# Kernel optimization log

Measured on AMD Instinct MI355X. Metric: run time of the kernel, lower is better.

## Reference

```python
import jax, jax.numpy as jnp
import numpy as np
from jax import lax

B, C, H, W = 4, 256, 64, 64
K = 9          # points
G = 32         # GroupNorm groups
EPS = 1e-5


def base_offset():
    # matches get_base_offset: y = 0, x in [-(K-1)//2 .. K//2], interleaved (y,x)
    bx = jnp.arange(-((K - 1) // 2), K // 2 + 1, dtype=jnp.float32)
    by = jnp.zeros_like(bx)
    return jnp.stack([by, bx], axis=1).reshape(1, 2 * K, 1, 1)


def conv3x3(x, w, b):
    y = lax.conv_general_dilated(x, w, (1, 1), ((1, 1), (1, 1)),
                                 dimension_numbers=('NCHW', 'OIHW', 'NCHW'))
    return y + b[None, :, None, None]


def group_norm(x, gamma, beta):
    b, c, h, w = x.shape
    xg = x.reshape(b, G, c // G, h, w)
    mu = xg.mean(axis=(2, 3, 4), keepdims=True)
    var = xg.var(axis=(2, 3, 4), keepdims=True)
    xn = ((xg - mu) * lax.rsqrt(var + EPS)).reshape(b, c, h, w)
    return xn * gamma[None, :, None, None] + beta[None, :, None, None]


def _deform_sample_one(img, off):
    # img: [C,H,W]; off: [K,2,H,W] (y,x). Kernel [1,K], stride 1, pad (0, K//2).
    c, h, w = img.shape
    base_x = (jnp.arange(K) - K // 2).astype(img.dtype)  # kernel grid x positions
    py = off[:, 0] + jnp.arange(h, dtype=img.dtype)[None, :, None]                 # [K,H,W]
    px = off[:, 1] + jnp.arange(w, dtype=img.dtype)[None, None, :] + base_x[:, None, None]
    y0 = jnp.floor(py)
    x0 = jnp.floor(px)
    wy = py - y0
    wx = px - x0
    flat = img.reshape(c, h * w)

    def corner(yi, xi):
        valid = (yi >= 0) & (yi <= h - 1) & (xi >= 0) & (xi <= w - 1)
        yc = jnp.clip(yi, 0, h - 1).astype(jnp.int32)
        xc = jnp.clip(xi, 0, w - 1).astype(jnp.int32)
        v = flat[:, (yc * w + xc).reshape(-1)].reshape(c, K, h, w)
        return v * valid[None].astype(img.dtype)

    return (corner(y0, x0) * ((1 - wy) * (1 - wx))[None]
            + corner(y0, x0 + 1) * ((1 - wy) * wx)[None]
            + corner(y0 + 1, x0) * (wy * (1 - wx))[None]
            + corner(y0 + 1, x0 + 1) * (wy * wx)[None])  # [C,K,H,W]


def deform_conv(x, offset, w):
    # x [B,C,H,W]; offset [B,2K,H,W]; w [O,C,1,K]; no bias (mmcv DeformConv2d)
    b, _, h, ww = x.shape
    off = offset.reshape(b, K, 2, h, ww)
    cols = jax.vmap(_deform_sample_one)(x, off)  # [B,C,K,H,W]
    return jnp.einsum('bckhw,ock->bohw', cols, w[:, :, 0, :])


def setup_inputs() -> dict:
    key = jax.random.key(0)
    ks = jax.random.split(key, 8)
    return {
        'cls_feat': jax.random.normal(ks[0], (B, C, H, W), jnp.float32),
        'reg_feat': jax.random.normal(ks[1], (B, C, H, W), jnp.float32),
        'offc_w': jax.random.normal(ks[2], (C, C, 3, 3), jnp.float32) * 0.01,
        'offc_b': jnp.zeros((C,), jnp.float32),
        'offc_g': jnp.ones((C,), jnp.float32),
        'offc_bt': jnp.zeros((C,), jnp.float32),
        'offo_w': jax.random.normal(ks[3], (2 * K, C, 3, 3), jnp.float32) * 0.01,
        'offo_b': jnp.zeros((2 * K,), jnp.float32),
        'clsdc_w': jax.random.normal(ks[4], (C, C, 1, K), jnp.float32) / np.sqrt(C * K),
        'cls_g': jnp.ones((C,), jnp.float32),
        'cls_bt': jnp.zeros((C,), jnp.float32),
        'regdc_w': jax.random.normal(ks[5], (C, C, 1, K), jnp.float32) / np.sqrt(C * K),
        'reg_g': jnp.ones((C,), jnp.float32),
        'reg_bt': jnp.zeros((C,), jnp.float32),
    }


def reference(cls_feat, reg_feat, offc_w, offc_b, offc_g, offc_bt,
              offo_w, offo_b, clsdc_w, cls_g, cls_bt, regdc_w, reg_g, reg_bt):
    # offset branch: ConvModule(3x3) -> GN -> ReLU, then 3x3 offset_out head
    t = jax.nn.relu(group_norm(conv3x3(reg_feat, offc_w, offc_b), offc_g, offc_bt))
    pts = conv3x3(t, offo_w, offo_b)          # [B, 2K, H, W]
    off = pts - base_offset()
    cls_out = jax.nn.relu(group_norm(deform_conv(cls_feat, off, clsdc_w), cls_g, cls_bt))
    reg_out = jax.nn.relu(group_norm(deform_conv(reg_feat, off, regdc_w), reg_g, reg_bt))
    return pts, cls_out, reg_out
```

## Files before the change

### kernel.cpp

```cpp
#include <hip/hip_runtime.h>
#include <math.h>

#define BB 4
#define CC 256
#define HH 64
#define WW 64
#define KP 9
#define GG 32
#define HWW (HH*WW)
#define FEL ((size_t)BB*CC*HH*WW)
#define GN_CNT 32768.0f

typedef __bf16 bf16x8 __attribute__((ext_vector_type(8)));
typedef float  f32x4  __attribute__((ext_vector_type(4)));

__device__ __forceinline__ float bflo(unsigned u) {
    union { unsigned u; float f; } x; x.u = u << 16; return x.f;
}
__device__ __forceinline__ float bfhi(unsigned u) {
    union { unsigned u; float f; } x; x.u = u & 0xffff0000u; return x.f;
}

#define VT256_RD(row, P)  (((row) << 8) + ((((P) ^ ((row) & 7))) << 3))
#define VT256_WR(row, u)  (((row) << 8) + (((((u) >> 1) ^ ((row) & 7))) << 3) + (((u) & 1) << 2))
#define VT128_RD(row, P)  (((row) << 7) + ((((P) ^ ((row) & 7))) << 3))
#define VT128_WR(row, u)  (((row) << 7) + (((((u) >> 1) ^ ((row) & 7))) << 3) + (((u) & 1) << 2))

__global__ void prep_all(const float* __restrict__ w1, const float* __restrict__ wc,
                         const float* __restrict__ wr, const float* __restrict__ w18,
                         __bf16* __restrict__ f1, __bf16* __restrict__ fc,
                         __bf16* __restrict__ fr, __bf16* __restrict__ f18,
                         float* __restrict__ stats) {
    int gid = blockIdx.x * 256 + threadIdx.x;
    if (gid < 768) stats[gid] = 0.f;
    const int NW = 589824;
    if (gid < 3 * NW) {
        int which = gid / NW;
        int idx = gid - which * NW;
        int j   = idx & 7;
        int l   = (idx >> 3) & 63;
        int o16 = (idx >> 9) & 15;
        int c0  = (idx >> 13) & 7;
        int k   = idx >> 16;
        int o = o16 * 16 + (l & 15);
        int c = c0 * 32 + (l >> 4) * 8 + j;
        const float* src = (which == 0) ? w1 : ((which == 1) ? wc : wr);
        __bf16* dst = (which == 0) ? f1 : ((which == 1) ? fc : fr);
        dst[idx] = (__bf16)src[(size_t)(o * 256 + c) * 9 + k];
    } else {
        int idx = gid - 3 * NW;
        int j   = idx & 7;
        int l   = (idx >> 3) & 63;
        int o16 = (idx >> 9) & 1;
        int c0  = (idx >> 10) & 7;
        int k   = idx >> 13;
        int o = o16 * 16 + (l & 15);
        int c = c0 * 32 + (l >> 4) * 8 + j;
        float v = (o < 18) ? w18[(size_t)(o * 256 + c) * 9 + k] : 0.f;
        f18[idx] = (__bf16)v;
    }
}

__global__ void transpose_feat(const float* __restrict__ cls,
                               const float* __restrict__ reg,
                               __bf16* __restrict__ out_cls,
                               __bf16* __restrict__ out_reg) {
    __shared__ float tile[64][65];
    int c0 = blockIdx.x * 64;
    int y  = blockIdx.y;
    int b  = blockIdx.z & 3;
    const float* in = (blockIdx.z >> 2) ? reg : cls;
    __bf16* out     = (blockIdx.z >> 2) ? out_reg : out_cls;
    int lx = threadIdx.x & 63;
    int q  = threadIdx.x >> 6;
    for (int j = 0; j < 16; ++j) {
        int ci = q * 16 + j;
        tile[ci][lx] = in[(((size_t)b*CC + c0 + ci)*HH + y)*WW + lx];
    }
    __syncthreads();
    for (int j = 0; j < 16; ++j) {
        int xi = q * 16 + j;
        out[(((size_t)b*HH + y)*WW + xi)*CC + c0 + lx] = (__bf16)tile[lx][xi];
    }
}

__global__ __launch_bounds__(256, 2) void conv1_mfma(
    const __bf16* __restrict__ in_cl,
    const __bf16* __restrict__ wf,
    const float* __restrict__ bias,
    __bf16* __restrict__ t_out,
    float* __restrict__ stats)
{
    __shared__ __bf16 Vt[66 * 256];
    __shared__ float groupStats[64];
    int blk = blockIdx.x;
    int bb = blk & 3;
    int oh = (blk >> 2) & 1;
    int y  = blk >> 3;
    int t  = threadIdx.x;
    int w  = t >> 6;
    int l  = t & 63;
    int quad = l >> 4;
    int l15  = l & 15;
    if (t < 64) groupStats[t] = 0.f;

    const __bf16* inb = in_cl + (size_t)bb * HWW * CC;
    f32x4 acc[4][2];
    #pragma unroll
    for (int i = 0; i < 4; ++i)
        #pragma unroll
        for (int j = 0; j < 2; ++j)
            acc[i][j] = (f32x4){0.f, 0.f, 0.f, 0.f};

    for (int ky = 0; ky < 3; ++ky) {
        int yy = y + ky - 1;
        bool yok = (yy >= 0 && yy < HH);
        __syncthreads();
        for (int u = t; u < 66 * 64; u += 256) {
            int xl = u >> 6, cu = u & 63;
            int gx = xl - 1;
            uint2 val = make_uint2(0u, 0u);
            if (yok && gx >= 0 && gx < WW)
                val = *(const uint2*)(inb + ((size_t)(yy * WW + gx)) * CC + cu * 4);
            *(uint2*)&Vt[VT256_WR(xl, cu)] = val;
        }
        __syncthreads();
        #pragma unroll
        for (int kx = 0; kx < 3; ++kx) {
            int k = ky * 3 + kx;
            const bf16x8* wbase = (const bf16x8*)(wf + (size_t)k * 65536);
            for (int c0 = 0; c0 < 8; ++c0) {
                bf16x8 a[4], bfr[2];
                #pragma unroll
                for (int pt = 0; pt < 4; ++pt) {
                    int row = pt * 16 + l15 + kx;
                    a[pt] = *(const bf16x8*)&Vt[VT256_RD(row, c0 * 4 + quad)];
                }
                #pragma unroll
                for (int ot = 0; ot < 2; ++ot)
                    bfr[ot] = wbase[(c0 * 16 + (oh * 8 + w * 2 + ot)) * 64 + l];
                #pragma unroll
                for (int pt = 0; pt < 4; ++pt)
                    #pragma unroll
                    for (int ot = 0; ot < 2; ++ot)
                        acc[pt][ot] = __builtin_amdgcn_mfma_f32_16x16x32_bf16(
                            a[pt], bfr[ot], acc[pt][ot], 0, 0, 0);
            }
        }
    }
    #pragma unroll
    for (int ot = 0; ot < 2; ++ot) {
        int o = oh * 128 + w * 32 + ot * 16 + l15;
        float bi = bias[o];
        float s1 = 0.f, s2 = 0.f;
        #pragma unroll
        for (int pt = 0; pt < 4; ++pt)
            #pragma unroll
            for (int r = 0; r < 4; ++r) {
                float v = acc[pt][ot][r] + bi;
                int px = pt * 16 + quad * 4 + r;
                t_out[(((size_t)bb * HH + y) * WW + px) * CC + o] = (__bf16)v;
                s1 += v; s2 += v * v;
            }
        s1 += __shfl_xor(s1, 16, 64); s1 += __shfl_xor(s1, 32, 64);
        s2 += __shfl_xor(s2, 16, 64); s2 += __shfl_xor(s2, 32, 64);
        if (quad == 0) {
            atomicAdd(&groupStats[(o >> 3) * 2],     s1);
            atomicAdd(&groupStats[(o >> 3) * 2 + 1], s2);
        }
    }
    __syncthreads();
    if (t < 64) atomicAdd(&stats[bb * 64 + t], groupStats[t]);
}

__global__ __launch_bounds__(256, 2) void conv18_mfma(
    const __bf16* __restrict__ t_bf,
    const __bf16* __restrict__ wf18,
    const float* __restrict__ bias,
    const float* __restrict__ stats,
    const float* __restrict__ gamma, const float* __restrict__ beta,
    float* __restrict__ pts)
{
    __shared__ __bf16 Vt[66 * 256];
    int blk = blockIdx.x;
    int bb = blk & 3;
    int y  = blk >> 2;
    int t  = threadIdx.x;
    int w  = t >> 6;
    int l  = t & 63;
    int quad = l >> 4;
    int l15  = l & 15;
    const __bf16* inb = t_bf + (size_t)bb * HWW * CC;

    int cbase = (t & 63) * 4;
    int g = cbase >> 3;
    float mu = stats[bb * 64 + g * 2]     * (1.f / GN_CNT);
    float ms = stats[bb * 64 + g * 2 + 1] * (1.f / GN_CNT);
    float rs = rsqrtf(ms - mu * mu + 1e-5f);
    float sc[4], sh[4];
    #pragma unroll
    for (int j = 0; j < 4; ++j) {
        float ga = gamma[cbase + j];
        sc[j] = rs * ga;
        sh[j] = beta[cbase + j] - mu * rs * ga;
    }

    f32x4 acc[2];
    acc[0] = (f32x4){0.f, 0.f, 0.f, 0.f};
    acc[1] = (f32x4){0.f, 0.f, 0.f, 0.f};

    for (int ky = 0; ky < 3; ++ky) {
        int yy = y + ky - 1;
        bool yok = (yy >= 0 && yy < HH);
        __syncthreads();
        for (int u = t; u < 66 * 64; u += 256) {
            int xl = u >> 6, cu = u & 63;
            int gx = xl - 1;
            uint2 val = make_uint2(0u, 0u);
            if (yok && gx >= 0 && gx < WW) {
                uint2 q = *(const uint2*)(inb + ((size_t)(yy * WW + gx)) * CC + cu * 4);
                float v0 = fmaxf(bflo(q.x) * sc[0] + sh[0], 0.f);
                float v1 = fmaxf(bfhi(q.x) * sc[1] + sh[1], 0.f);
                float v2 = fmaxf(bflo(q.y) * sc[2] + sh[2], 0.f);
                float v3 = fmaxf(bfhi(q.y) * sc[3] + sh[3], 0.f);
                __bf16 o4[4] = {(__bf16)v0, (__bf16)v1, (__bf16)v2, (__bf16)v3};
                val = *(const uint2*)o4;
            }
            *(uint2*)&Vt[VT256_WR(xl, cu)] = val;
        }
        __syncthreads();
        #pragma unroll
        for (int kx = 0; kx < 3; ++kx) {
            int k = ky * 3 + kx;
            const bf16x8* wbase = (const bf16x8*)(wf18 + (size_t)k * 8192);
            for (int c0 = 0; c0 < 8; ++c0) {
                int row = w * 16 + l15 + kx;
                bf16x8 a = *(const bf16x8*)&Vt[VT256_RD(row, c0 * 4 + quad)];
                #pragma unroll
                for (int o16 = 0; o16 < 2; ++o16) {
                    bf16x8 bfr = wbase[(c0 * 2 + o16) * 64 + l];
                    acc[o16] = __builtin_amdgcn_mfma_f32_16x16x32_bf16(a, bfr, acc[o16], 0, 0, 0);
                }
            }
        }
    }
    #pragma unroll
    for (int o16 = 0; o16 < 2; ++o16) {
        int o = o16 * 16 + l15;
        if (o < 18) {
            float bi = bias[o];
            float4 st;
            st.x = acc[o16][0] + bi;
            st.y = acc[o16][1] + bi;
            st.z = acc[o16][2] + bi;
            st.w = acc[o16][3] + bi;
            *(float4*)(pts + (((size_t)bb*18 + o)*HH + y)*WW + w*16 + quad*4) = st;
        }
    }
}

__global__ __launch_bounds__(256, 2) void deform_mfma(
    const __bf16* __restrict__ cls_cl, const __bf16* __restrict__ reg_cl,
    const __bf16* __restrict__ wfc, const __bf16* __restrict__ wfr,
    const float* __restrict__ pts,
    __bf16* __restrict__ out_cls, __bf16* __restrict__ out_reg,
    float* __restrict__ stats)
{
    __shared__ float pairW4[576 * 4];
    __shared__ int   pairO4[576 * 4];
    __shared__ __bf16 Vt[2][64 * 128];
    __shared__ float groupStats[64];

    int blk = blockIdx.x;
    int g8  = blk & 7;
    int which = g8 & 1;
    int bb  = g8 >> 1;
    int y   = blk >> 3;
    const __bf16* featb = (which ? reg_cl : cls_cl) + (size_t)bb * HWW * CC;
    const __bf16* wf    = which ? wfr : wfc;
    __bf16* outp  = which ? out_reg : out_cls;
    float* statsP = stats + 256 + which * 256 + bb * 64;

    int t = threadIdx.x;
    int w = t >> 6;
    int l = t & 63;
    int quad = l >> 4;
    int l15  = l & 15;
    int lh   = l >> 5;
    int cq   = l & 31;

    if (t < 64) groupStats[t] = 0.f;
    for (int j = t; j < 576; j += 256) {
        int k = j >> 6;
        int x = j & 63;
        float py  = pts[(((size_t)bb*18 + 2*k)*HH + y)*WW + x] + (float)y;
        float pxf = pts[(((size_t)bb*18 + 2*k + 1)*HH + y)*WW + x] + (float)x;
        float y0f = floorf(py), x0f = floorf(pxf);
        float wy = py - y0f, wx = pxf - x0f;
        int iy0 = (int)y0f, ix0 = (int)x0f;
        int iy1 = iy0 + 1,  ix1 = ix0 + 1;
        bool vy0 = (iy0 >= 0 && iy0 < HH), vy1 = (iy1 >= 0 && iy1 < HH);
        bool vx0 = (ix0 >= 0 && ix0 < WW), vx1 = (ix1 >= 0 && ix1 < WW);
        int cy0 = min(max(iy0, 0), HH-1), cy1 = min(max(iy1, 0), HH-1);
        int cx0 = min(max(ix0, 0), WW-1), cx1 = min(max(ix1, 0), WW-1);
        pairW4[j*4+0] = (1.f-wy)*(1.f-wx) * ((vy0 && vx0) ? 1.f : 0.f);
        pairW4[j*4+1] = (1.f-wy)*wx       * ((vy0 && vx1) ? 1.f : 0.f);
        pairW4[j*4+2] = wy*(1.f-wx)       * ((vy1 && vx0) ? 1.f : 0.f);
        pairW4[j*4+3] = wy*wx             * ((vy1 && vx1) ? 1.f : 0.f);
        pairO4[j*4+0] = (cy0*WW + cx0)*CC;
        pairO4[j*4+1] = (cy0*WW + cx1)*CC;
        pairO4[j*4+2] = (cy1*WW + cx0)*CC;
        pairO4[j*4+3] = (cy1*WW + cx1)*CC;
    }

    f32x4 acc[4][4];
    #pragma unroll
    for (int i = 0; i < 4; ++i)
        #pragma unroll
        for (int j = 0; j < 4; ++j)
            acc[i][j] = (f32x4){0.f, 0.f, 0.f, 0.f};

    auto sample2 = [&](int s, int u) {
        int k = s >> 1, ch = s & 1;
        __bf16* buf = &Vt[s & 1][0];
        const __bf16* fb = featb + ch * 128 + cq * 4;
        #pragma unroll
        for (int it2 = 0; it2 < 2; ++it2) {
            int pxi = w * 16 + (u * 2 + it2) * 2 + lh;
            int j = k * 64 + pxi;
            float4 wv = *(const float4*)&pairW4[j * 4];
            int4   ov = *(const int4*)&pairO4[j * 4];
            uint2 q00 = *(const uint2*)(fb + ov.x);
            uint2 q01 = *(const uint2*)(fb + ov.y);
            uint2 q10 = *(const uint2*)(fb + ov.z);
            uint2 q11 = *(const uint2*)(fb + ov.w);
            float v0 = wv.x*bflo(q00.x) + wv.y*bflo(q01.x) + wv.z*bflo(q10.x) + wv.w*bflo(q11.x);
            float v1 = wv.x*bfhi(q00.x) + wv.y*bfhi(q01.x) + wv.z*bfhi(q10.x) + wv.w*bfhi(q11.x);
            float v2 = wv.x*bflo(q00.y) + wv.y*bflo(q01.y) + wv.z*bflo(q10.y) + wv.w*bflo(q11.y);
            float v3 = wv.x*bfhi(q00.y) + wv.y*bfhi(q01.y) + wv.z*bfhi(q10.y) + wv.w*bfhi(q11.y);
            __bf16 o4[4] = {(__bf16)v0, (__bf16)v1, (__bf16)v2, (__bf16)v3};
            *(uint2*)&buf[VT128_WR(pxi, cq)] = *(const uint2*)o4;
        }
    };
    auto mfma4 = [&](int s, int u) {
        int k = s >> 1, ch = s & 1;
        const __bf16* buf = &Vt[s & 1][0];
        const bf16x8* wbase = (const bf16x8*)(wf + (size_t)k * 65536);
        int c0g = ch * 4 + u;
        bf16x8 a[4], bfr[4];
        #pragma unroll
        for (int pt = 0; pt < 4; ++pt)
            a[pt] = *(const bf16x8*)&buf[VT128_RD(pt * 16 + l15, u * 4 + quad)];
        #pragma unroll
        for (int ot = 0; ot < 4; ++ot)
            bfr[ot] = wbase[(c0g * 16 + (w * 4 + ot)) * 64 + l];
        #pragma unroll
        for (int ot = 0; ot < 4; ++ot)
            #pragma unroll
            for (int pt = 0; pt < 4; ++pt)
                acc[ot][pt] = __builtin_amdgcn_mfma_f32_16x16x32_bf16(
                    bfr[ot], a[pt], acc[ot][pt], 0, 0, 0);
    };

    __syncthreads();
    #pragma unroll
    for (int u = 0; u < 4; ++u) sample2(0, u);
    #pragma unroll 1
    for (int s = 1; s < 18; ++s) {
        __syncthreads();
        #pragma unroll
        for (int u = 0; u < 4; ++u) {
            sample2(s, u);
            mfma4(s - 1, u);
        }
    }
    __syncthreads();
    #pragma unroll
    for (int u = 0; u < 4; ++u) mfma4(17, u);

    #pragma unroll
    for (int ot = 0; ot < 4; ++ot)
        #pragma unroll
        for (int r = 0; r < 4; ++r) {
            int o = w * 64 + ot * 16 + quad * 4 + r;
            __bf16* orow = outp + ((size_t)(bb*CC + o))*HWW + y*WW + l15;
            float s1 = 0.f, s2 = 0.f;
            #pragma unroll
            for (int pt = 0; pt < 4; ++pt) {
                float v = acc[ot][pt][r];
                orow[pt * 16] = (__bf16)v;
                s1 += v; s2 += v * v;
            }
            s1 += __shfl_xor(s1, 1, 64); s1 += __shfl_xor(s1, 2, 64);
            s1 += __shfl_xor(s1, 4, 64); s1 += __shfl_xor(s1, 8, 64);
            s2 += __shfl_xor(s2, 1, 64); s2 += __shfl_xor(s2, 2, 64);
            s2 += __shfl_xor(s2, 4, 64); s2 += __shfl_xor(s2, 8, 64);
            if (l15 == 0) {
                atomicAdd(&groupStats[(o >> 3) * 2],     s1);
                atomicAdd(&groupStats[(o >> 3) * 2 + 1], s2);
            }
        }
    __syncthreads();
    if (t < 64) atomicAdd(&statsP[t], groupStats[t]);
}

__global__ void gn_relu_nchw(const __bf16* __restrict__ in_cls, const __bf16* __restrict__ in_reg,
                             float* __restrict__ out_cls, float* __restrict__ out_reg,
                             const float* __restrict__ stats_base,
                             const float* __restrict__ gcls, const float* __restrict__ bcls,
                             const float* __restrict__ greg, const float* __restrict__ breg) {
    int which = blockIdx.y;
    const __bf16* in = which ? in_reg  : in_cls;
    float* out       = which ? out_reg : out_cls;
    const float* st  = stats_base + (which ? 512 : 256);
    const float* gg  = which ? greg : gcls;
    const float* be  = which ? breg : bcls;
    size_t e = ((size_t)blockIdx.x * 256 + threadIdx.x) * 8;
    int c = (int)((e >> 12) & 255);
    int b = (int)(e >> 20);
    int g = c >> 3;
    float mu = st[(b*32 + g)*2] * (1.f / GN_CNT);
    float ms = st[(b*32 + g)*2 + 1] * (1.f / GN_CNT);
    float rs = rsqrtf(ms - mu*mu + 1e-5f);
    float ga = gg[c], bb = be[c];
    uint4 q = *(const uint4*)(in + e);
    float v[8] = {bflo(q.x), bfhi(q.x), bflo(q.y), bfhi(q.y),
                  bflo(q.z), bfhi(q.z), bflo(q.w), bfhi(q.w)};
    float4 r0, r1;
    r0.x = fmaxf((v[0] - mu)*rs*ga + bb, 0.f);
    r0.y = fmaxf((v[1] - mu)*rs*ga + bb, 0.f);
    r0.z = fmaxf((v[2] - mu)*rs*ga + bb, 0.f);
    r0.w = fmaxf((v[3] - mu)*rs*ga + bb, 0.f);
    r1.x = fmaxf((v[4] - mu)*rs*ga + bb, 0.f);
    r1.y = fmaxf((v[5] - mu)*rs*ga + bb, 0.f);
    r1.z = fmaxf((v[6] - mu)*rs*ga + bb, 0.f);
    r1.w = fmaxf((v[7] - mu)*rs*ga + bb, 0.f);
    *(float4*)(out + e)     = r0;
    *(float4*)(out + e + 4) = r1;
}

extern "C" void kernel_launch(void* const* d_in, const int* in_sizes, int n_in,
                              void* d_out, int out_size, void* d_ws, size_t ws_size,
                              hipStream_t stream) {
    (void)in_sizes; (void)n_in; (void)out_size; (void)ws_size;
    const float* cls_feat = (const float*)d_in[0];
    const float* reg_feat = (const float*)d_in[1];
    const float* offc_w   = (const float*)d_in[2];
    const float* offc_b   = (const float*)d_in[3];
    const float* offc_g   = (const float*)d_in[4];
    const float* offc_bt  = (const float*)d_in[5];
    const float* offo_w   = (const float*)d_in[6];
    const float* offo_b   = (const float*)d_in[7];
    const float* clsdc_w  = (const float*)d_in[8];
    const float* cls_g    = (const float*)d_in[9];
    const float* cls_bt   = (const float*)d_in[10];
    const float* regdc_w  = (const float*)d_in[11];
    const float* reg_g    = (const float*)d_in[12];
    const float* reg_bt   = (const float*)d_in[13];
    float* out = (float*)d_out;

    char* ws = (char*)d_ws;
    __bf16* reg_cl = (__bf16*)ws;
    __bf16* cls_cl = (__bf16*)(ws + 8388608);
    __bf16* t_bf   = (__bf16*)(ws + 16777216);
    __bf16* dc_cls = (__bf16*)(ws + 25165824);
    __bf16* dc_reg = (__bf16*)(ws + 33554432);
    __bf16* wt1f   = (__bf16*)(ws + 41943040);
    __bf16* wtcf   = (__bf16*)(ws + 41943040 + 1179648);
    __bf16* wtrf   = (__bf16*)(ws + 41943040 + 2359296);
    __bf16* wf18   = (__bf16*)(ws + 41943040 + 3538944);
    float*  stats  = (float*)(ws + 41943040 + 3686400);

    float* pts     = out;
    float* out_cls = out + 294912;
    float* out_reg = out + 294912 + FEL;

    hipLaunchKernelGGL(prep_all, dim3(7200), dim3(256), 0, stream,
                       offc_w, clsdc_w, regdc_w, offo_w, wt1f, wtcf, wtrf, wf18, stats);
    hipLaunchKernelGGL(transpose_feat, dim3(4, 64, 8), dim3(256), 0, stream,
                       cls_feat, reg_feat, cls_cl, reg_cl);
    hipLaunchKernelGGL(conv1_mfma, dim3(512), dim3(256), 0, stream,
                       reg_cl, wt1f, offc_b, t_bf, stats);
    hipLaunchKernelGGL(conv18_mfma, dim3(256), dim3(256), 0, stream,
                       t_bf, wf18, offo_b, stats, offc_g, offc_bt, pts);
    hipLaunchKernelGGL(deform_mfma, dim3(512), dim3(256), 0, stream,
                       cls_cl, reg_cl, wtcf, wtrf, pts, dc_cls, dc_reg, stats);
    hipLaunchKernelGGL(gn_relu_nchw, dim3(2048, 2), dim3(256), 0, stream,
                       dc_cls, dc_reg, out_cls, out_reg,
                       stats, cls_g, cls_bt, reg_g, reg_bt);
}
```

Measured before the change: 282.1 us.

## Split conv and deform kernels across more blocks/waves and software-pipeline deform gathers

Conv1 now gives each block one 64-channel output quarter instead of a half, doubling the grid and cutting accumulators so occupancy can rise. Conv18 splits each row into two 32-pixel halves with a smaller LDS tile. The deform kernel moves to 512 threads, with each wave owning 32 output channels. Its sampling is restructured so all gather loads for the next stage are issued before the MFMAs of the current stage, to hide gather latency. In exchange, weight fragments are reloaded across more blocks and more registers are held live for the prefetched gathers.

```diff
diff --git a/kernel.cpp b/kernel.cpp
--- a/kernel.cpp
+++ b/kernel.cpp
@@ -84,7 +84,7 @@
     }
 }
 
-__global__ __launch_bounds__(256, 2) void conv1_mfma(
+__global__ __launch_bounds__(256, 4) void conv1_mfma(
     const __bf16* __restrict__ in_cl,
     const __bf16* __restrict__ wf,
     const float* __restrict__ bias,
@@ -95,8 +95,8 @@
     __shared__ float groupStats[64];
     int blk = blockIdx.x;
     int bb = blk & 3;
-    int oh = (blk >> 2) & 1;
-    int y  = blk >> 3;
+    int oq = (blk >> 2) & 3;
+    int y  = blk >> 4;
     int t  = threadIdx.x;
     int w  = t >> 6;
     int l  = t & 63;
@@ -105,12 +105,9 @@
     if (t < 64) groupStats[t] = 0.f;
 
     const __bf16* inb = in_cl + (size_t)bb * HWW * CC;
-    f32x4 acc[4][2];
+    f32x4 acc[4];
     #pragma unroll
-    for (int i = 0; i < 4; ++i)
-        #pragma unroll
-        for (int j = 0; j < 2; ++j)
-            acc[i][j] = (f32x4){0.f, 0.f, 0.f, 0.f};
+    for (int i = 0; i < 4; ++i) acc[i] = (f32x4){0.f, 0.f, 0.f, 0.f};
 
     for (int ky = 0; ky < 3; ++ky) {
         int yy = y + ky - 1;
@@ -130,34 +127,29 @@
             int k = ky * 3 + kx;
             const bf16x8* wbase = (const bf16x8*)(wf + (size_t)k * 65536);
             for (int c0 = 0; c0 < 8; ++c0) {
-                bf16x8 a[4], bfr[2];
+                bf16x8 a[4];
                 #pragma unroll
                 for (int pt = 0; pt < 4; ++pt) {
                     int row = pt * 16 + l15 + kx;
                     a[pt] = *(const bf16x8*)&Vt[VT256_RD(row, c0 * 4 + quad)];
                 }
-                #pragma unroll
-                for (int ot = 0; ot < 2; ++ot)
-                    bfr[ot] = wbase[(c0 * 16 + (oh * 8 + w * 2 + ot)) * 64 + l];
+                bf16x8 bfr = wbase[(c0 * 16 + (oq * 4 + w)) * 64 + l];
                 #pragma unroll
                 for (int pt = 0; pt < 4; ++pt)
-                    #pragma unroll
-                    for (int ot = 0; ot < 2; ++ot)
-                        acc[pt][ot] = __builtin_amdgcn_mfma_f32_16x16x32_bf16(
-                            a[pt], bfr[ot], acc[pt][ot], 0, 0, 0);
-            }
-        }
-    }
-    #pragma unroll
-    for (int ot = 0; ot < 2; ++ot) {
-        int o = oh * 128 + w * 32 + ot * 16 + l15;
+                    acc[pt] = __builtin_amdgcn_mfma_f32_16x16x32_bf16(
+                        a[pt], bfr, acc[pt], 0, 0, 0);
+            }
+        }
+    }
+    {
+        int o = oq * 64 + w * 16 + l15;
         float bi = bias[o];
         float s1 = 0.f, s2 = 0.f;
         #pragma unroll
         for (int pt = 0; pt < 4; ++pt)
             #pragma unroll
             for (int r = 0; r < 4; ++r) {
-                float v = acc[pt][ot][r] + bi;
+                float v = acc[pt][r] + bi;
                 int px = pt * 16 + quad * 4 + r;
                 t_out[(((size_t)bb * HH + y) * WW + px) * CC + o] = (__bf16)v;
                 s1 += v; s2 += v * v;
@@ -173,7 +165,7 @@
     if (t < 64) atomicAdd(&stats[bb * 64 + t], groupStats[t]);
 }
 
-__global__ __launch_bounds__(256, 2) void conv18_mfma(
+__global__ __launch_bounds__(256, 4) void conv18_mfma(
     const __bf16* __restrict__ t_bf,
     const __bf16* __restrict__ wf18,
     const float* __restrict__ bias,
@@ -181,15 +173,19 @@
     const float* __restrict__ gamma, const float* __restrict__ beta,
     float* __restrict__ pts)
 {
-    __shared__ __bf16 Vt[66 * 256];
+    __shared__ __bf16 Vt[34 * 256];
     int blk = blockIdx.x;
     int bb = blk & 3;
-    int y  = blk >> 2;
+    int xh = (blk >> 2) & 1;
+    int y  = blk >> 3;
     int t  = threadIdx.x;
     int w  = t >> 6;
     int l  = t & 63;
     int quad = l >> 4;
     int l15  = l & 15;
+    int mt   = w & 1;
+    int o16  = w >> 1;
+    int x0   = xh * 32;
     const __bf16* inb = t_bf + (size_t)bb * HWW * CC;
 
     int cbase = (t & 63) * 4;
@@ -205,17 +201,15 @@
         sh[j] = beta[cbase + j] - mu * rs * ga;
     }
 
-    f32x4 acc[2];
-    acc[0] = (f32x4){0.f, 0.f, 0.f, 0.f};
-    acc[1] = (f32x4){0.f, 0.f, 0.f, 0.f};
+    f32x4 acc = (f32x4){0.f, 0.f, 0.f, 0.f};
 
     for (int ky = 0; ky < 3; ++ky) {
         int yy = y + ky - 1;
         bool yok = (yy >= 0 && yy < HH);
         __syncthreads();
-        for (int u = t; u < 66 * 64; u += 256) {
+        for (int u = t; u < 34 * 64; u += 256) {
             int xl = u >> 6, cu = u & 63;
-            int gx = xl - 1;
+            int gx = x0 - 1 + xl;
             uint2 val = make_uint2(0u, 0u);
             if (yok && gx >= 0 && gx < WW) {
                 uint2 q = *(const uint2*)(inb + ((size_t)(yy * WW + gx)) * CC + cu * 4);
@@ -234,32 +228,28 @@
             int k = ky * 3 + kx;
             const bf16x8* wbase = (const bf16x8*)(wf18 + (size_t)k * 8192);
             for (int c0 = 0; c0 < 8; ++c0) {
-                int row = w * 16 + l15 + kx;
+                int row = mt * 16 + l15 + kx;
                 bf16x8 a = *(const bf16x8*)&Vt[VT256_RD(row, c0 * 4 + quad)];
-                #pragma unroll
-                for (int o16 = 0; o16 < 2; ++o16) {
-                    bf16x8 bfr = wbase[(c0 * 2 + o16) * 64 + l];
-                    acc[o16] = __builtin_amdgcn_mfma_f32_16x16x32_bf16(a, bfr, acc[o16], 0, 0, 0);
-                }
-            }
-        }
-    }
-    #pragma unroll
-    for (int o16 = 0; o16 < 2; ++o16) {
+                bf16x8 bfr = wbase[(c0 * 2 + o16) * 64 + l];
+                acc = __builtin_amdgcn_mfma_f32_16x16x32_bf16(a, bfr, acc, 0, 0, 0);
+            }
+        }
+    }
+    {
         int o = o16 * 16 + l15;
         if (o < 18) {
             float bi = bias[o];
             float4 st;
-            st.x = acc[o16][0] + bi;
-            st.y = acc[o16][1] + bi;
-            st.z = acc[o16][2] + bi;
-            st.w = acc[o16][3] + bi;
-            *(float4*)(pts + (((size_t)bb*18 + o)*HH + y)*WW + w*16 + quad*4) = st;
-        }
-    }
-}
-
-__global__ __launch_bounds__(256, 2) void deform_mfma(
+            st.x = acc[0] + bi;
+            st.y = acc[1] + bi;
+            st.z = acc[2] + bi;
+            st.w = acc[3] + bi;
+            *(float4*)(pts + (((size_t)bb*18 + o)*HH + y)*WW + x0 + mt*16 + quad*4) = st;
+        }
+    }
+}
+
+__global__ __launch_bounds__(512, 4) void deform_mfma(
     const __bf16* __restrict__ cls_cl, const __bf16* __restrict__ reg_cl,
     const __bf16* __restrict__ wfc, const __bf16* __restrict__ wfr,
     const float* __restrict__ pts,
@@ -286,11 +276,11 @@
     int l = t & 63;
     int quad = l >> 4;
     int l15  = l & 15;
-    int lh   = l >> 5;
-    int cq   = l & 31;
+    int tp   = t >> 5;
+    int cq   = t & 31;
 
     if (t < 64) groupStats[t] = 0.f;
-    for (int j = t; j < 576; j += 256) {
+    for (int j = t; j < 576; j += 512) {
         int k = j >> 6;
         int x = j & 63;
         float py  = pts[(((size_t)bb*18 + 2*k)*HH + y)*WW + x] + (float)y;
@@ -313,76 +303,87 @@
         pairO4[j*4+3] = (cy1*WW + cx1)*CC;
     }
 
-    f32x4 acc[4][4];
+    f32x4 acc[2][4];
     #pragma unroll
-    for (int i = 0; i < 4; ++i)
+    for (int i = 0; i < 2; ++i)
         #pragma unroll
         for (int j = 0; j < 4; ++j)
             acc[i][j] = (f32x4){0.f, 0.f, 0.f, 0.f};
 
-    auto sample2 = [&](int s, int u) {
+    auto stage_loads = [&](int s, uint2 L[4][4], float4 WV[4]) {
         int k = s >> 1, ch = s & 1;
+        const __bf16* fb = featb + ch * 128 + cq * 4;
+        #pragma unroll
+        for (int it = 0; it < 4; ++it) {
+            int pxi = it * 16 + tp;
+            int j = k * 64 + pxi;
+            WV[it] = *(const float4*)&pairW4[j * 4];
+            int4 ov = *(const int4*)&pairO4[j * 4];
+            L[it][0] = *(const uint2*)(fb + ov.x);
+            L[it][1] = *(const uint2*)(fb + ov.y);
+            L[it][2] = *(const uint2*)(fb + ov.z);
+            L[it][3] = *(const uint2*)(fb + ov.w);
+        }
+    };
+    auto stage_combine = [&](int s, uint2 L[4][4], float4 WV[4]) {
         __bf16* buf = &Vt[s & 1][0];
-        const __bf16* fb = featb + ch * 128 + cq * 4;
-        #pragma unroll
-        for (int it2 = 0; it2 < 2; ++it2) {
-            int pxi = w * 16 + (u * 2 + it2) * 2 + lh;
-            int j = k * 64 + pxi;
-            float4 wv = *(const float4*)&pairW4[j * 4];
-            int4   ov = *(const int4*)&pairO4[j * 4];
-            uint2 q00 = *(const uint2*)(fb + ov.x);
-            uint2 q01 = *(const uint2*)(fb + ov.y);
-            uint2 q10 = *(const uint2*)(fb + ov.z);
-            uint2 q11 = *(const uint2*)(fb + ov.w);
-            float v0 = wv.x*bflo(q00.x) + wv.y*bflo(q01.x) + wv.z*bflo(q10.x) + wv.w*bflo(q11.x);
-            float v1 = wv.x*bfhi(q00.x) + wv.y*bfhi(q01.x) + wv.z*bfhi(q10.x) + wv.w*bfhi(q11.x);
-            float v2 = wv.x*bflo(q00.y) + wv.y*bflo(q01.y) + wv.z*bflo(q10.y) + wv.w*bflo(q11.y);
-            float v3 = wv.x*bfhi(q00.y) + wv.y*bfhi(q01.y) + wv.z*bfhi(q10.y) + wv.w*bfhi(q11.y);
+        #pragma unroll
+        for (int it = 0; it < 4; ++it) {
+            int pxi = it * 16 + tp;
+            float4 wv = WV[it];
+            float v0 = wv.x*bflo(L[it][0].x) + wv.y*bflo(L[it][1].x) + wv.z*bflo(L[it][2].x) + wv.w*bflo(L[it][3].x);
+            float v1 = wv.x*bfhi(L[it][0].x) + wv.y*bfhi(L[it][1].x) + wv.z*bfhi(L[it][2].x) + wv.w*bfhi(L[it][3].x);
+            float v2 = wv.x*bflo(L[it][0].y) + wv.y*bflo(L[it][1].y) + wv.z*bflo(L[it][2].y) + wv.w*bflo(L[it][3].y);
+            float v3 = wv.x*bfhi(L[it][0].y) + wv.y*bfhi(L[it][1].y) + wv.z*bfhi(L[it][2].y) + wv.w*bfhi(L[it][3].y);
             __bf16 o4[4] = {(__bf16)v0, (__bf16)v1, (__bf16)v2, (__bf16)v3};
             *(uint2*)&buf[VT128_WR(pxi, cq)] = *(const uint2*)o4;
         }
     };
-    auto mfma4 = [&](int s, int u) {
+    auto stage_mfma = [&](int s) {
         int k = s >> 1, ch = s & 1;
         const __bf16* buf = &Vt[s & 1][0];
         const bf16x8* wbase = (const bf16x8*)(wf + (size_t)k * 65536);
-        int c0g = ch * 4 + u;
-        bf16x8 a[4], bfr[4];
-        #pragma unroll
-        for (int pt = 0; pt < 4; ++pt)
-            a[pt] = *(const bf16x8*)&buf[VT128_RD(pt * 16 + l15, u * 4 + quad)];
-        #pragma unroll
-        for (int ot = 0; ot < 4; ++ot)
-            bfr[ot] = wbase[(c0g * 16 + (w * 4 + ot)) * 64 + l];
-        #pragma unroll
-        for (int ot = 0; ot < 4; ++ot)
+        #pragma unroll
+        for (int u = 0; u < 4; ++u) {
+            int c0g = ch * 4 + u;
+            bf16x8 a[4], bfr[2];
             #pragma unroll
             for (int pt = 0; pt < 4; ++pt)
-                acc[ot][pt] = __builtin_amdgcn_mfma_f32_16x16x32_bf16(
-                    bfr[ot], a[pt], acc[ot][pt], 0, 0, 0);
+                a[pt] = *(const bf16x8*)&buf[VT128_RD(pt * 16 + l15, u * 4 + quad)];
+            #pragma unroll
+            for (int ot = 0; ot < 2; ++ot)
+                bfr[ot] = wbase[(c0g * 16 + (w * 2 + ot)) * 64 + l];
+            #pragma unroll
+            for (int ot = 0; ot < 2; ++ot)
+                #pragma unroll
+                for (int pt = 0; pt < 4; ++pt)
+                    acc[ot][pt] = __builtin_amdgcn_mfma_f32_16x16x32_bf16(
+                        bfr[ot], a[pt], acc[ot][pt], 0, 0, 0);
+        }
     };
 
     __syncthreads();
-    #pragma unroll
-    for (int u = 0; u < 4; ++u) sample2(0, u);
+    {
+        uint2 L[4][4]; float4 WV[4];
+        stage_loads(0, L, WV);
+        stage_combine(0, L, WV);
+    }
     #pragma unroll 1
     for (int s = 1; s < 18; ++s) {
         __syncthreads();
-        #pragma unroll
-        for (int u = 0; u < 4; ++u) {
-            sample2(s, u);
-            mfma4(s - 1, u);
-        }
+        uint2 L[4][4]; float4 WV[4];
+        stage_loads(s, L, WV);
+        stage_mfma(s - 1);
+        stage_combine(s, L, WV);
     }
     __syncthreads();
+    stage_mfma(17);
+
     #pragma unroll
-    for (int u = 0; u < 4; ++u) mfma4(17, u);
-
-    #pragma unroll
-    for (int ot = 0; ot < 4; ++ot)
+    for (int ot = 0; ot < 2; ++ot)
         #pragma unroll
         for (int r = 0; r < 4; ++r) {
-            int o = w * 64 + ot * 16 + quad * 4 + r;
+            int o = w * 32 + ot * 16 + quad * 4 + r;
             __bf16* orow = outp + ((size_t)(bb*CC + o))*HWW + y*WW + l15;
             float s1 = 0.f, s2 = 0.f;
             #pragma unroll
@@ -479,11 +480,11 @@
                        offc_w, clsdc_w, regdc_w, offo_w, wt1f, wtcf, wtrf, wf18, stats);
     hipLaunchKernelGGL(transpose_feat, dim3(4, 64, 8), dim3(256), 0, stream,
                        cls_feat, reg_feat, cls_cl, reg_cl);
-    hipLaunchKernelGGL(conv1_mfma, dim3(512), dim3(256), 0, stream,
+    hipLaunchKernelGGL(conv1_mfma, dim3(1024), dim3(256), 0, stream,
                        reg_cl, wt1f, offc_b, t_bf, stats);
-    hipLaunchKernelGGL(conv18_mfma, dim3(256), dim3(256), 0, stream,
+    hipLaunchKernelGGL(conv18_mfma, dim3(512), dim3(256), 0, stream,
                        t_bf, wf18, offo_b, stats, offc_g, offc_bt, pts);
-    hipLaunchKernelGGL(deform_mfma, dim3(512), dim3(256), 0, stream,
+    hipLaunchKernelGGL(deform_mfma, dim3(512), dim3(512), 0, stream,
                        cls_cl, reg_cl, wtcf, wtrf, pts, dc_cls, dc_reg, stats);
     hipLaunchKernelGGL(gn_relu_nchw, dim3(2048, 2), dim3(256), 0, stream,
                        dc_cls, dc_reg, out_cls, out_reg,
```

Measured after the change: 255.3 us. 1.11x faster.
